# Kernel tuning notes

Hardware: AMD Instinct MI355X
Metric: run time of the kernel (lower is better)

## Reference

```python
import jax, jax.numpy as jnp
import numpy as np

N_NODES = 500000
N_EDGES = 5000000


def _sage_conv(x, edge_index, Wl, bl, Wr):
    # PyG SAGEConv (aggr='mean', root_weight=True):
    #   out = lin_l(mean_{j in N(i)} x_j) + lin_r(x_i)
    # edge_index[0] = source, edge_index[1] = target
    src, dst = edge_index[0], edge_index[1]
    n = x.shape[0]
    msg = x[src]  # [E, F] gather
    agg = jax.ops.segment_sum(msg, dst, num_segments=n)  # [N, F]
    deg = jax.ops.segment_sum(jnp.ones((src.shape[0],), x.dtype), dst, num_segments=n)
    agg = agg / jnp.maximum(deg, 1.0)[:, None]  # mean aggregation
    return agg @ Wl.T + bl + x @ Wr.T


def setup_inputs() -> dict:
    key = jax.random.key(0)
    k1, k2, k3, k4, k5, k6 = jax.random.split(key, 6)
    x = jax.random.normal(k1, (N_NODES, 2), dtype=jnp.float32)
    edge_index = jax.random.randint(k2, (2, N_EDGES), 0, N_NODES, dtype=jnp.int64)
    # conv1: SAGEConv(2, 16); conv2: SAGEConv(16, 1)
    s1 = 1.0 / np.sqrt(2.0)
    s2 = 1.0 / np.sqrt(16.0)
    W1l = jax.random.uniform(k3, (16, 2), jnp.float32, -s1, s1)
    W1r = jax.random.uniform(k4, (16, 2), jnp.float32, -s1, s1)
    b1 = jnp.zeros((16,), jnp.float32)
    W2l = jax.random.uniform(k5, (1, 16), jnp.float32, -s2, s2)
    W2r = jax.random.uniform(k6, (1, 16), jnp.float32, -s2, s2)
    b2 = jnp.zeros((1,), jnp.float32)
    return {"x": x, "edge_index": edge_index,
            "W1l": W1l, "b1": b1, "W1r": W1r,
            "W2l": W2l, "b2": b2, "W2r": W2r}


def reference(x, edge_index, W1l, b1, W1r, W2l, b2, W2r):
    h = jax.nn.relu(_sage_conv(x, edge_index, W1l, b1, W1r))  # [N, 16]
    h = _sage_conv(h, edge_index, W2l, b2, W2r)               # [N, 1]
    return jax.nn.sigmoid(h).squeeze(-1)                      # [N]
```

## Files before the change

kernel.cpp:

```cpp
#include <hip/hip_runtime.h>


static constexpr int ABLOCK = 512;
static constexpr int PBLOCK = 1024;
static constexpr int PGRID = 256;
static constexpr int BUCKET_BITS = 10;
static constexpr int BUCKET_NODES = 1 << BUCKET_BITS;
static constexpr int CAP = 16384;
static constexpr int CSTRIDE = 16;
static constexpr int MAXCHUNK = 19584;

static constexpr float S1 = 65536.0f;
static constexpr float IS1 = 1.0f / 65536.0f;
static constexpr long long B1 = 8LL * 65536LL;
static constexpr float S2 = 16384.0f;
static constexpr float IS2 = 1.0f / 16384.0f;
static constexpr int   B2 = 128 * 16384;

__global__ __launch_bounds__(512) void k_init(unsigned* __restrict__ cursor, int NB) {
    int b = blockIdx.x * 512 + threadIdx.x;
    if (b < NB) cursor[(size_t)b * CSTRIDE] = (unsigned)b * (unsigned)CAP;
}

__global__ __launch_bounds__(PBLOCK) void k_part(
    const int* __restrict__ src, const int* __restrict__ dst,
    unsigned* __restrict__ cursor, unsigned* __restrict__ entries,
    int E, int NB)
{
    __shared__ unsigned sorted[MAXCHUNK];
    __shared__ unsigned hist[512];
    __shared__ unsigned loc[512];
    __shared__ unsigned base[512];
    const int tid = threadIdx.x;
    const int chunk = (E + gridDim.x - 1) / gridDim.x;
    const int e0 = blockIdx.x * chunk;
    const int e1 = min(e0 + chunk, E);
    const int n = e1 - e0;
    const int nv = n >> 2;
    const int4* dst4 = reinterpret_cast<const int4*>(dst + e0);
    const int4* src4 = reinterpret_cast<const int4*>(src + e0);

    for (int b = tid; b < 512; b += PBLOCK) hist[b] = 0;
    __syncthreads();

    for (int t = tid; t < nv; t += PBLOCK) {
        int4 d = dst4[t];
        atomicAdd(&hist[(unsigned)d.x >> BUCKET_BITS], 1u);
        atomicAdd(&hist[(unsigned)d.y >> BUCKET_BITS], 1u);
        atomicAdd(&hist[(unsigned)d.z >> BUCKET_BITS], 1u);
        atomicAdd(&hist[(unsigned)d.w >> BUCKET_BITS], 1u);
    }
    for (int e = e0 + (nv << 2) + tid; e < e1; e += PBLOCK)
        atomicAdd(&hist[(unsigned)dst[e] >> BUCKET_BITS], 1u);
    __syncthreads();

    if (tid < NB) loc[tid] = hist[tid];
    __syncthreads();
    for (int off = 1; off < NB; off <<= 1) {
        unsigned v = 0;
        if (tid < NB && tid >= off) v = loc[tid - off];
        __syncthreads();
        if (tid < NB) loc[tid] += v;
        __syncthreads();
    }
    if (tid < NB) loc[tid] -= hist[tid];

    if (tid < NB) {
        int b = tid + (int)(blockIdx.x % (unsigned)NB);
        if (b >= NB) b -= NB;
        base[b] = atomicAdd(&cursor[(size_t)b * CSTRIDE], hist[b]);
    }
    __syncthreads();
    for (int b = tid; b < 512; b += PBLOCK) hist[b] = 0;
    __syncthreads();

    for (int t = tid; t < nv; t += PBLOCK) {
        int4 d = dst4[t];
        int4 s = src4[t];
        {
            unsigned bk = (unsigned)d.x >> BUCKET_BITS;
            unsigned r = atomicAdd(&hist[bk], 1u);
            sorted[loc[bk] + r] = ((unsigned)s.x << BUCKET_BITS) | ((unsigned)d.x & (BUCKET_NODES - 1));
        }
        {
            unsigned bk = (unsigned)d.y >> BUCKET_BITS;
            unsigned r = atomicAdd(&hist[bk], 1u);
            sorted[loc[bk] + r] = ((unsigned)s.y << BUCKET_BITS) | ((unsigned)d.y & (BUCKET_NODES - 1));
        }
        {
            unsigned bk = (unsigned)d.z >> BUCKET_BITS;
            unsigned r = atomicAdd(&hist[bk], 1u);
            sorted[loc[bk] + r] = ((unsigned)s.z << BUCKET_BITS) | ((unsigned)d.z & (BUCKET_NODES - 1));
        }
        {
            unsigned bk = (unsigned)d.w >> BUCKET_BITS;
            unsigned r = atomicAdd(&hist[bk], 1u);
            sorted[loc[bk] + r] = ((unsigned)s.w << BUCKET_BITS) | ((unsigned)d.w & (BUCKET_NODES - 1));
        }
    }
    for (int e = e0 + (nv << 2) + tid; e < e1; e += PBLOCK) {
        unsigned d = (unsigned)dst[e];
        unsigned bk = d >> BUCKET_BITS;
        unsigned r = atomicAdd(&hist[bk], 1u);
        sorted[loc[bk] + r] = ((unsigned)src[e] << BUCKET_BITS) | (d & (BUCKET_NODES - 1));
    }
    __syncthreads();

    const int wave = tid >> 6, lane = tid & 63;
    const int nw = PBLOCK >> 6;
    const int off = (int)(blockIdx.x % (unsigned)NB);
    for (int j = wave; j < NB; j += nw) {
        int b = j + off;
        if (b >= NB) b -= NB;
        unsigned cnt = hist[b];
        if (cnt == 0) continue;
        unsigned lo = loc[b], ba = base[b];
        unsigned lim = (unsigned)(b + 1) * (unsigned)CAP;
        if (ba >= lim) continue;
        cnt = min(cnt, lim - ba);
        for (unsigned i = lane; i < cnt; i += 64)
            entries[ba + i] = sorted[lo + i];
    }
}

__global__ __launch_bounds__(ABLOCK) void k_agg1(
    const unsigned* __restrict__ entries, const unsigned* __restrict__ cursor,
    const float* __restrict__ x,
    const float* __restrict__ W1l, const float* __restrict__ b1,
    const float* __restrict__ W1r, const float* __restrict__ W2l,
    const float* __restrict__ W2r, const float* __restrict__ b2,
    unsigned* __restrict__ sq, float* __restrict__ t0a, float* __restrict__ inva,
    unsigned* __restrict__ dega, int N)
{
    __shared__ unsigned long long qs[BUCKET_NODES];
    int bk = blockIdx.x;
    for (int i = threadIdx.x; i < BUCKET_NODES; i += ABLOCK) qs[i] = 0ULL;
    __syncthreads();

    unsigned start = (unsigned)bk * (unsigned)CAP;
    unsigned end = min(cursor[(size_t)bk * CSTRIDE], start + (unsigned)CAP);
    unsigned n = end - start;
    unsigned nv = n >> 2;
    const uint4* e4 = reinterpret_cast<const uint4*>(entries + start);

    #define PROC1(en) { \
        unsigned s_ = (en) >> BUCKET_BITS; \
        unsigned dl_ = (en) & (BUCKET_NODES - 1); \
        float2 xv_ = *reinterpret_cast<const float2*>(x + 2 * (size_t)s_); \
        unsigned q0_ = (unsigned)__float2int_rn((xv_.x + 8.0f) * S1); \
        unsigned q1_ = (unsigned)__float2int_rn((xv_.y + 8.0f) * S1); \
        atomicAdd(&qs[dl_], (1ULL << 56) | ((unsigned long long)q0_ << 28) | (unsigned long long)q1_); }

    for (unsigned t = threadIdx.x; t < nv; t += ABLOCK) {
        uint4 en = e4[t];
        PROC1(en.x) PROC1(en.y) PROC1(en.z) PROC1(en.w)
    }
    for (unsigned t = start + (nv << 2) + threadIdx.x; t < end; t += ABLOCK) {
        unsigned en = entries[t];
        PROC1(en)
    }
    #undef PROC1
    __syncthreads();

    int nodebase = bk << BUCKET_BITS;
    for (int il = threadIdx.x; il < BUCKET_NODES; il += ABLOCK) {
        int i = nodebase + il;
        if (i >= N) continue;
        unsigned long long v = qs[il];
        int deg = (int)(v >> 56);
        long long q0 = (long long)((v >> 28) & 0xFFFFFFFULL);
        long long q1 = (long long)(v & 0xFFFFFFFULL);
        long long bias = (long long)deg * B1;
        float inv = 1.0f / (float)max(deg, 1);
        float m0 = (float)(q0 - bias) * IS1 * inv;
        float m1 = (float)(q1 - bias) * IS1 * inv;
        float2 xv = *reinterpret_cast<const float2*>(x + 2 * (size_t)i);
        float s = 0.0f, t0 = b2[0];
#pragma unroll
        for (int o = 0; o < 16; ++o) {
            float h = m0 * W1l[2 * o] + m1 * W1l[2 * o + 1] + b1[o]
                    + xv.x * W1r[2 * o] + xv.y * W1r[2 * o + 1];
            h = fmaxf(h, 0.0f);
            s  += h * W2l[o];
            t0 += h * W2r[o];
        }
        sq[i]   = (unsigned)__float2int_rn((s + 128.0f) * S2);
        t0a[i]  = t0;
        inva[i] = inv;
        dega[i] = (unsigned)deg;
    }
}

__global__ __launch_bounds__(ABLOCK) void k_agg2(
    const unsigned* __restrict__ entries, const unsigned* __restrict__ cursor,
    const unsigned* __restrict__ sq,
    const float* __restrict__ t0a, const float* __restrict__ inva,
    const unsigned* __restrict__ dega,
    float* __restrict__ out, int N)
{
    __shared__ unsigned sbin[BUCKET_NODES];
    int bk = blockIdx.x;
    for (int i = threadIdx.x; i < BUCKET_NODES; i += ABLOCK) sbin[i] = 0;
    __syncthreads();

    unsigned start = (unsigned)bk * (unsigned)CAP;
    unsigned end = min(cursor[(size_t)bk * CSTRIDE], start + (unsigned)CAP);
    unsigned n = end - start;
    unsigned nv = n >> 2;
    const uint4* e4 = reinterpret_cast<const uint4*>(entries + start);

    #define PROC2(en) { \
        unsigned s_ = (en) >> BUCKET_BITS; \
        unsigned dl_ = (en) & (BUCKET_NODES - 1); \
        atomicAdd(&sbin[dl_], sq[s_]); }

    for (unsigned t = threadIdx.x; t < nv; t += ABLOCK) {
        uint4 en = e4[t];
        PROC2(en.x) PROC2(en.y) PROC2(en.z) PROC2(en.w)
    }
    for (unsigned t = start + (nv << 2) + threadIdx.x; t < end; t += ABLOCK) {
        unsigned en = entries[t];
        PROC2(en)
    }
    #undef PROC2
    __syncthreads();

    int nodebase = bk << BUCKET_BITS;
    for (int il = threadIdx.x; il < BUCKET_NODES; il += ABLOCK) {
        int i = nodebase + il;
        if (i >= N) continue;
        int deg = (int)dega[i];
        float mean_s = (float)((int)sbin[il] - deg * B2) * IS2 * inva[i];
        out[i] = 1.0f / (1.0f + expf(-(mean_s + t0a[i])));
    }
}

__global__ __launch_bounds__(256) void k_scatter1_fb(
    const int* __restrict__ src, const int* __restrict__ dst,
    const float* __restrict__ x, float* __restrict__ agg1, float* __restrict__ deg, int E)
{
    int stride = gridDim.x * blockDim.x;
    for (int e = blockIdx.x * blockDim.x + threadIdx.x; e < E; e += stride) {
        int s = src[e], d = dst[e];
        float2 xv = *reinterpret_cast<const float2*>(x + 2 * (size_t)s);
        unsafeAtomicAdd(&agg1[2 * (size_t)d + 0], xv.x);
        unsafeAtomicAdd(&agg1[2 * (size_t)d + 1], xv.y);
        unsafeAtomicAdd(&deg[d], 1.0f);
    }
}
__global__ __launch_bounds__(256) void k_node1_fb(
    const float* __restrict__ x, const float* __restrict__ agg1, const float* __restrict__ deg,
    const float* __restrict__ W1l, const float* __restrict__ b1,
    const float* __restrict__ W1r, const float* __restrict__ W2l,
    float* __restrict__ sval, int N)
{
    int i = blockIdx.x * blockDim.x + threadIdx.x;
    if (i >= N) return;
    float inv = 1.0f / fmaxf(deg[i], 1.0f);
    float2 a = *reinterpret_cast<const float2*>(agg1 + 2 * (size_t)i);
    float m0 = a.x * inv, m1 = a.y * inv;
    float2 xv = *reinterpret_cast<const float2*>(x + 2 * (size_t)i);
    float s = 0.0f;
#pragma unroll
    for (int o = 0; o < 16; ++o) {
        float h = m0 * W1l[2 * o] + m1 * W1l[2 * o + 1] + b1[o]
                + xv.x * W1r[2 * o] + xv.y * W1r[2 * o + 1];
        s += fmaxf(h, 0.0f) * W2l[o];
    }
    sval[i] = s;
}
__global__ __launch_bounds__(256) void k_scatter2_fb(
    const int* __restrict__ src, const int* __restrict__ dst,
    const float* __restrict__ sval, float* __restrict__ agg_s, int E)
{
    int stride = gridDim.x * blockDim.x;
    for (int e = blockIdx.x * blockDim.x + threadIdx.x; e < E; e += stride)
        unsafeAtomicAdd(&agg_s[dst[e]], sval[src[e]]);
}
__global__ __launch_bounds__(256) void k_node2_fb(
    const float* __restrict__ x, const float* __restrict__ agg1, const float* __restrict__ deg,
    const float* __restrict__ agg_s,
    const float* __restrict__ W1l, const float* __restrict__ b1,
    const float* __restrict__ W1r, const float* __restrict__ W2r, const float* __restrict__ b2,
    float* __restrict__ out, int N)
{
    int i = blockIdx.x * blockDim.x + threadIdx.x;
    if (i >= N) return;
    float inv = 1.0f / fmaxf(deg[i], 1.0f);
    float2 a = *reinterpret_cast<const float2*>(agg1 + 2 * (size_t)i);
    float m0 = a.x * inv, m1 = a.y * inv;
    float2 xv = *reinterpret_cast<const float2*>(x + 2 * (size_t)i);
    float t = agg_s[i] * inv + b2[0];
#pragma unroll
    for (int o = 0; o < 16; ++o) {
        float h = m0 * W1l[2 * o] + m1 * W1l[2 * o + 1] + b1[o]
                + xv.x * W1r[2 * o] + xv.y * W1r[2 * o + 1];
        t += fmaxf(h, 0.0f) * W2r[o];
    }
    out[i] = 1.0f / (1.0f + expf(-t));
}

extern "C" void kernel_launch(void* const* d_in, const int* in_sizes, int n_in,
                              void* d_out, int out_size, void* d_ws, size_t ws_size,
                              hipStream_t stream) {
    const float* x   = (const float*)d_in[0];
    const int*   ei  = (const int*)d_in[1];
    const float* W1l = (const float*)d_in[2];
    const float* b1  = (const float*)d_in[3];
    const float* W1r = (const float*)d_in[4];
    const float* W2l = (const float*)d_in[5];
    const float* b2  = (const float*)d_in[6];
    const float* W2r = (const float*)d_in[7];

    const int N = in_sizes[0] / 2;
    const int E = in_sizes[1] / 2;
    const int* src = ei;
    const int* dst = ei + (size_t)E;
    float* out = (float*)d_out;

    const int NB = (N + BUCKET_NODES - 1) >> BUCKET_BITS;
    const int chunk = (E + PGRID - 1) / PGRID;

    size_t needed = 512 * CSTRIDE * 4 + (size_t)NB * CAP * 4 + 4 * (size_t)N * 4;
    if (NB <= 512 && chunk <= MAXCHUNK && ws_size >= needed) {
        unsigned* cursor  = (unsigned*)d_ws;
        unsigned* entries = cursor + 512 * CSTRIDE;
        unsigned* sq      = entries + (size_t)NB * CAP;
        float*    t0a     = (float*)(sq + N);
        float*    inva    = t0a + N;
        unsigned* dega    = (unsigned*)(inva + N);

        k_init<<<(NB + 511) / 512, 512, 0, stream>>>(cursor, NB);
        k_part<<<PGRID, PBLOCK, 0, stream>>>(src, dst, cursor, entries, E, NB);
        k_agg1<<<NB, ABLOCK, 0, stream>>>(entries, cursor, x, W1l, b1, W1r, W2l, W2r, b2,
                                          sq, t0a, inva, dega, N);
        k_agg2<<<NB, ABLOCK, 0, stream>>>(entries, cursor, sq, t0a, inva, dega, out, N);
    } else {
        float* agg1  = (float*)d_ws;
        float* deg   = agg1 + 2 * (size_t)N;
        float* agg_s = deg + (size_t)N;
        float* sval  = agg_s + (size_t)N;
        hipMemsetAsync(d_ws, 0, 4 * (size_t)N * sizeof(float), stream);
        const int eblocks = 2048, nblocks = (N + 255) / 256;
        k_scatter1_fb<<<eblocks, 256, 0, stream>>>(src, dst, x, agg1, deg, E);
        k_node1_fb<<<nblocks, 256, 0, stream>>>(x, agg1, deg, W1l, b1, W1r, W2l, sval, N);
        k_scatter2_fb<<<eblocks, 256, 0, stream>>>(src, dst, sval, agg_s, E);
        k_node2_fb<<<nblocks, 256, 0, stream>>>(x, agg1, deg, agg_s, W1l, b1, W1r, W2r, b2, out, N);
    }
}
```

Before: 94.99 us.

## Halve bucket size to 512 nodes and fold degree bias into per-node scale

Shrinks destination buckets from 1024 to 512 nodes, so the node count gives about 977 buckets and twice as many aggregation blocks with smaller shared bins. Capacity per bucket is halved to match, and the partition arrays grow to 1024 entries. Phase 2 now precomputes a combined scale and a bias-adjusted t0 per node, removing the deg and inv arrays and one global read stream. Risks include more partition scatter segments per block, a more costly prefix scan over 1024 buckets, and bucket overflow when CAP drops to 8192.

```diff
diff --git a/kernel.cpp b/kernel.cpp
--- a/kernel.cpp
+++ b/kernel.cpp
@@ -4,9 +4,10 @@
 static constexpr int ABLOCK = 512;
 static constexpr int PBLOCK = 1024;
 static constexpr int PGRID = 256;
-static constexpr int BUCKET_BITS = 10;
+static constexpr int BUCKET_BITS = 9;
 static constexpr int BUCKET_NODES = 1 << BUCKET_BITS;
-static constexpr int CAP = 16384;
+static constexpr int MAXNB = 1024;
+static constexpr int CAP = 8192;
 static constexpr int CSTRIDE = 16;
 static constexpr int MAXCHUNK = 19584;
 
@@ -15,7 +16,6 @@
 static constexpr long long B1 = 8LL * 65536LL;
 static constexpr float S2 = 16384.0f;
 static constexpr float IS2 = 1.0f / 16384.0f;
-static constexpr int   B2 = 128 * 16384;
 
 __global__ __launch_bounds__(512) void k_init(unsigned* __restrict__ cursor, int NB) {
     int b = blockIdx.x * 512 + threadIdx.x;
@@ -28,19 +28,19 @@
     int E, int NB)
 {
     __shared__ unsigned sorted[MAXCHUNK];
-    __shared__ unsigned hist[512];
-    __shared__ unsigned loc[512];
-    __shared__ unsigned base[512];
+    __shared__ unsigned hist[MAXNB];
+    __shared__ unsigned loc[MAXNB];
+    __shared__ unsigned base[MAXNB];
     const int tid = threadIdx.x;
-    const int chunk = (E + gridDim.x - 1) / gridDim.x;
+    int chunk = ((E + (int)gridDim.x - 1) / (int)gridDim.x + 3) & ~3;
     const int e0 = blockIdx.x * chunk;
     const int e1 = min(e0 + chunk, E);
-    const int n = e1 - e0;
+    const int n = max(0, e1 - e0);
     const int nv = n >> 2;
     const int4* dst4 = reinterpret_cast<const int4*>(dst + e0);
     const int4* src4 = reinterpret_cast<const int4*>(src + e0);
 
-    for (int b = tid; b < 512; b += PBLOCK) hist[b] = 0;
+    for (int b = tid; b < MAXNB; b += PBLOCK) hist[b] = 0;
     __syncthreads();
 
     for (int t = tid; t < nv; t += PBLOCK) {
@@ -71,7 +71,7 @@
         base[b] = atomicAdd(&cursor[(size_t)b * CSTRIDE], hist[b]);
     }
     __syncthreads();
-    for (int b = tid; b < 512; b += PBLOCK) hist[b] = 0;
+    for (int b = tid; b < MAXNB; b += PBLOCK) hist[b] = 0;
     __syncthreads();
 
     for (int t = tid; t < nv; t += PBLOCK) {
@@ -129,8 +129,8 @@
     const float* __restrict__ W1l, const float* __restrict__ b1,
     const float* __restrict__ W1r, const float* __restrict__ W2l,
     const float* __restrict__ W2r, const float* __restrict__ b2,
-    unsigned* __restrict__ sq, float* __restrict__ t0a, float* __restrict__ inva,
-    unsigned* __restrict__ dega, int N)
+    unsigned* __restrict__ sq, float* __restrict__ t0a, float* __restrict__ ga,
+    int N)
 {
     __shared__ unsigned long long qs[BUCKET_NODES];
     int bk = blockIdx.x;
@@ -184,18 +184,16 @@
             s  += h * W2l[o];
             t0 += h * W2r[o];
         }
-        sq[i]   = (unsigned)__float2int_rn((s + 128.0f) * S2);
-        t0a[i]  = t0;
-        inva[i] = inv;
-        dega[i] = (unsigned)deg;
+        sq[i]  = (unsigned)__float2int_rn((s + 128.0f) * S2);
+        t0a[i] = t0 - (deg > 0 ? 128.0f : 0.0f);
+        ga[i]  = IS2 * inv;
     }
 }
 
 __global__ __launch_bounds__(ABLOCK) void k_agg2(
     const unsigned* __restrict__ entries, const unsigned* __restrict__ cursor,
     const unsigned* __restrict__ sq,
-    const float* __restrict__ t0a, const float* __restrict__ inva,
-    const unsigned* __restrict__ dega,
+    const float* __restrict__ t0a, const float* __restrict__ ga,
     float* __restrict__ out, int N)
 {
     __shared__ unsigned sbin[BUCKET_NODES];
@@ -229,9 +227,8 @@
     for (int il = threadIdx.x; il < BUCKET_NODES; il += ABLOCK) {
         int i = nodebase + il;
         if (i >= N) continue;
-        int deg = (int)dega[i];
-        float mean_s = (float)((int)sbin[il] - deg * B2) * IS2 * inva[i];
-        out[i] = 1.0f / (1.0f + expf(-(mean_s + t0a[i])));
+        float t = (float)(int)sbin[il] * ga[i] + t0a[i];
+        out[i] = 1.0f / (1.0f + expf(-t));
     }
 }
 
@@ -319,22 +316,21 @@
     float* out = (float*)d_out;
 
     const int NB = (N + BUCKET_NODES - 1) >> BUCKET_BITS;
-    const int chunk = (E + PGRID - 1) / PGRID;
-
-    size_t needed = 512 * CSTRIDE * 4 + (size_t)NB * CAP * 4 + 4 * (size_t)N * 4;
-    if (NB <= 512 && chunk <= MAXCHUNK && ws_size >= needed) {
+    const int chunk = ((E + PGRID - 1) / PGRID + 3) & ~3;
+
+    size_t needed = (size_t)MAXNB * CSTRIDE * 4 + (size_t)NB * CAP * 4 + 3 * (size_t)N * 4;
+    if (NB <= MAXNB && chunk <= MAXCHUNK && ws_size >= needed) {
         unsigned* cursor  = (unsigned*)d_ws;
-        unsigned* entries = cursor + 512 * CSTRIDE;
+        unsigned* entries = cursor + (size_t)MAXNB * CSTRIDE;
         unsigned* sq      = entries + (size_t)NB * CAP;
         float*    t0a     = (float*)(sq + N);
-        float*    inva    = t0a + N;
-        unsigned* dega    = (unsigned*)(inva + N);
+        float*    ga      = t0a + N;
 
         k_init<<<(NB + 511) / 512, 512, 0, stream>>>(cursor, NB);
         k_part<<<PGRID, PBLOCK, 0, stream>>>(src, dst, cursor, entries, E, NB);
         k_agg1<<<NB, ABLOCK, 0, stream>>>(entries, cursor, x, W1l, b1, W1r, W2l, W2r, b2,
-                                          sq, t0a, inva, dega, N);
-        k_agg2<<<NB, ABLOCK, 0, stream>>>(entries, cursor, sq, t0a, inva, dega, out, N);
+                                          sq, t0a, ga, N);
+        k_agg2<<<NB, ABLOCK, 0, stream>>>(entries, cursor, sq, t0a, ga, out, N);
     } else {
         float* agg1  = (float*)d_ws;
         float* deg   = agg1 + 2 * (size_t)N;
```

After: 111.2 us. +17.1%, slower.
